# Optimization experiments

Hardware: AMD Instinct MI355X
Metric: run time of the kernel (lower is better)

Reference implementation:

```python
import jax, jax.numpy as jnp
import numpy as np

NB = 8  # num_blocks

def setup_inputs() -> dict:
    key = jax.random.key(0)
    ks = jax.random.split(key, 8)
    C = 128
    C8 = C // 8
    s = 0.05
    x = jax.random.normal(ks[0], (1, C, 64, 64, 64), dtype=jnp.float32)
    Wq = jax.random.normal(ks[1], (C8, C), dtype=jnp.float32) * s
    bq = jax.random.normal(ks[2], (C8,), dtype=jnp.float32) * s
    Wk = jax.random.normal(ks[3], (C8, C), dtype=jnp.float32) * s
    bk = jax.random.normal(ks[4], (C8,), dtype=jnp.float32) * s
    Wv = jax.random.normal(ks[5], (C, C), dtype=jnp.float32) * s
    bv = jax.random.normal(ks[6], (C,), dtype=jnp.float32) * s
    # torch inits gamma=0 (output == x, zero grads through attention);
    # use 0.5 so the attention path is actually exercised.
    gamma = jnp.full((1,), 0.5, dtype=jnp.float32)
    return dict(x=x, Wq=Wq, bq=bq, Wk=Wk, bk=bk, Wv=Wv, bv=bv, gamma=gamma)

def reference(x, Wq, bq, Wk, bk, Wv, bv, gamma):
    B, C, D, H, W = x.shape
    db, hb, wb = D // NB, H // NB, W // NB
    n = db * hb * wb
    # (i, j, k, B, C, db, hb, wb) block layout
    xr = x.reshape(B, C, NB, db, NB, hb, NB, wb).transpose(2, 4, 6, 0, 1, 3, 5, 7)
    ar = jnp.arange(NB)
    # NOTE: original code computes k = i % num_blocks, i.e. k == i always.
    # Only the (i, j, i) diagonal blocks are attended; the rest stay zero in `out`.
    blk = xr[ar, :, ar].reshape(NB * NB * B, C, n)  # (P, C, n), P = NB*NB*B
    # 1x1x1 convs == per-voxel linear layers over channels
    q = jnp.einsum('pcn,dc->pdn', blk, Wq) + bq[None, :, None]  # (P, C/8, n)
    k = jnp.einsum('pcn,dc->pdn', blk, Wk) + bk[None, :, None]  # (P, C/8, n)
    v = jnp.einsum('pcn,dc->pdn', blk, Wv) + bv[None, :, None]  # (P, C,   n)
    attn = jax.nn.softmax(jnp.einsum('pdn,pdm->pnm', q, k), axis=-1)  # (P, n_q, n_k)
    ob = jnp.einsum('pdm,pnm->pdn', v, attn)  # value @ attn^T, (P, C, n)
    ob = ob.reshape(NB, NB, B, C, db, hb, wb)
    out = jnp.zeros_like(xr).at[ar, :, ar].set(ob)  # only k==i diagonal filled
    out = out.transpose(3, 4, 0, 5, 1, 6, 2, 7).reshape(B, C, D, H, W)
    return gamma * out + x
```

## Files before the change

### kernel.cpp

```cpp
#include <hip/hip_runtime.h>

typedef __attribute__((ext_vector_type(8))) short bf16x8;
typedef __attribute__((ext_vector_type(4))) float f32x4;
typedef __attribute__((ext_vector_type(4))) int i32x4;
typedef __attribute__((ext_vector_type(4))) float float4v;

#define MFMA16(a, b, c) __builtin_amdgcn_mfma_f32_16x16x32_bf16((a), (b), (c), 0, 0, 0)

__device__ __forceinline__ unsigned short f2bf(float f) {
    unsigned u = __builtin_bit_cast(unsigned, f);
    u += 0x7fffu + ((u >> 16) & 1u);
    return (unsigned short)(u >> 16);
}
__device__ __forceinline__ float bf2f(unsigned short s) {
    unsigned u = ((unsigned)s) << 16;
    return __builtin_bit_cast(float, u);
}
__device__ __forceinline__ int pkbf(float a, float b) {
    return (int)f2bf(a) | ((int)f2bf(b) << 16);
}


__global__ __launch_bounds__(512, 2) void battn_kernel(
    const float* __restrict__ x,
    const float* __restrict__ Wq, const float* __restrict__ bq,
    const float* __restrict__ Wk, const float* __restrict__ bk,
    const float* __restrict__ Wv, const float* __restrict__ bv,
    const float* __restrict__ gamma, float* __restrict__ out)
{
    __shared__ __attribute__((aligned(128))) char smem[159744];
    const int bid = blockIdx.x;
    const int tid = threadIdx.x;

    if (bid >= 64) {
        const float4v* __restrict__ xin = (const float4v*)x;
        float4v* __restrict__ o4 = (float4v*)out;
        const int total = 1 << 23;
        for (int u = (bid - 64) * 512 + tid; u < total; u += 384 * 512) {
            if ((((u >> 1) ^ (u >> 13)) & 7) != 0) {
                o4[u] = xin[u];
            }
        }
        return;
    }

    const int p = bid;
    const int ib = p >> 3, jb = p & 7;
    const int vbase = ib * 8 * 4096 + jb * 8 * 64 + ib * 8;
    const int lane = tid & 63, wv = tid >> 6;
    const int g = lane >> 4, c15 = lane & 15;

    for (int it = 0; it < 32; ++it) {
        int ch = it * 512 + tid;
        int c = ch >> 7;
        int m = (ch & 127) * 4;
        int vox = ((m >> 6) << 12) + (((m >> 3) & 7) << 6) + (m & 7);
        float4v v = *(const float4v*)(x + c * 262144 + vbase + vox);
        char* bp = smem + ((m * 256 + 2 * c) ^ (((m >> 2) & 7) << 4));
        *(unsigned short*)(bp)       = f2bf(v[0]);
        *(unsigned short*)(bp + 256) = f2bf(v[1]);
        *(unsigned short*)(bp + 512) = f2bf(v[2]);
        *(unsigned short*)(bp + 768) = f2bf(v[3]);
    }

    bf16x8 wqf[4], wkf[4], wvf[4];
    #pragma unroll
    for (int ks = 0; ks < 4; ++ks) {
        const float* sq = Wq + c15 * 128 + ks * 32 + g * 8;
        const float* sk = Wk + c15 * 128 + ks * 32 + g * 8;
        const float* sv = Wv + (wv * 16 + c15) * 128 + ks * 32 + g * 8;
        #pragma unroll
        for (int e = 0; e < 8; ++e) {
            wqf[ks][e] = (short)f2bf(sq[e]);
            wkf[ks][e] = (short)f2bf(sk[e]);
            wvf[ks][e] = (short)f2bf(sv[e]);
        }
    }
    const float bqv = bq[c15], bkv = bk[c15];
    const f32x4 zacc = {0.f, 0.f, 0.f, 0.f};
    const bf16x8 zfrag = (bf16x8)(short)0;

    __syncthreads();

    #pragma unroll
    for (int qi = 0; qi < 4; ++qi) {
        f32x4 acc = zacc;
        int mrow = wv * 64 + qi * 16 + c15;
        int sw = ((mrow >> 2) & 7) << 4;
        #pragma unroll
        for (int ks = 0; ks < 4; ++ks) {
            bf16x8 af = *(const bf16x8*)(smem + ((mrow * 256 + ks * 64 + g * 16) ^ sw));
            acc = MFMA16(af, wqf[ks], acc);
        }
        #pragma unroll
        for (int r = 0; r < 4; ++r) {
            int nql = qi * 16 + g * 4 + r;
            *(unsigned short*)(smem + 131072 + wv * 2048 + nql * 32 + 2 * c15) = f2bf(acc[r] + bqv);
        }
    }
    __syncthreads();
    bf16x8 qf[4];
    #pragma unroll
    for (int t = 0; t < 4; ++t) {
        bf16x8 v = zfrag;
        if (g < 2) v = *(const bf16x8*)(smem + 131072 + wv * 2048 + (t * 16 + c15) * 32 + g * 16);
        qf[t] = v;
    }
    __syncthreads();

    #pragma unroll
    for (int qi = 0; qi < 4; ++qi) {
        f32x4 acc = zacc;
        int mrow = wv * 64 + qi * 16 + c15;
        int sw = ((mrow >> 2) & 7) << 4;
        #pragma unroll
        for (int ks = 0; ks < 4; ++ks) {
            bf16x8 af = *(const bf16x8*)(smem + ((mrow * 256 + ks * 64 + g * 16) ^ sw));
            acc = MFMA16(af, wkf[ks], acc);
        }
        #pragma unroll
        for (int r = 0; r < 4; ++r) {
            int mk = wv * 64 + qi * 16 + g * 4 + r;
            *(unsigned short*)(smem + 131072 + mk * 32 + 2 * c15) = f2bf(acc[r] + bkv);
        }
    }
    __syncthreads();

    f32x4 o[4][8];
    #pragma unroll
    for (int t = 0; t < 4; ++t)
        #pragma unroll
        for (int ci = 0; ci < 8; ++ci)
            o[t][ci] = zacc;
    float lsum[4] = {0.f, 0.f, 0.f, 0.f};

    for (int kt = 0; kt < 16; ++kt) {
        int mk0 = kt * 32;
        #pragma unroll
        for (int mi = 0; mi < 2; ++mi) {
            f32x4 acc = zacc;
            int mrow = mk0 + mi * 16 + c15;
            int sw = ((mrow >> 2) & 7) << 4;
            #pragma unroll
            for (int ks = 0; ks < 4; ++ks) {
                bf16x8 bf = *(const bf16x8*)(smem + ((mrow * 256 + ks * 64 + g * 16) ^ sw));
                acc = MFMA16(wvf[ks], bf, acc);
            }
            #pragma unroll
            for (int r = 0; r < 4; ++r) {
                int c_out = wv * 16 + g * 4 + r;
                *(unsigned short*)(smem + 147456 + c_out * 80 + 2 * (mi * 16 + c15)) = f2bf(acc[r]);
            }
        }
        __syncthreads();

        bf16x8 ka[2];
        #pragma unroll
        for (int ki = 0; ki < 2; ++ki) {
            bf16x8 v = zfrag;
            if (g < 2) v = *(const bf16x8*)(smem + 131072 + (mk0 + ki * 16 + c15) * 32 + g * 16);
            ka[ki] = v;
        }

        bf16x8 pa[4];
        #pragma unroll
        for (int t = 0; t < 4; ++t) {
            f32x4 s0 = MFMA16(ka[0], qf[t], zacc);
            f32x4 s1 = MFMA16(ka[1], qf[t], zacc);
            float e00 = __expf(s0[0]), e01 = __expf(s0[1]), e02 = __expf(s0[2]), e03 = __expf(s0[3]);
            float e10 = __expf(s1[0]), e11 = __expf(s1[1]), e12 = __expf(s1[2]), e13 = __expf(s1[3]);
            lsum[t] += (e00 + e01) + (e02 + e03) + ((e10 + e11) + (e12 + e13));
            int wA0 = pkbf(e00, e01), wB0 = pkbf(e02, e03);
            int wA1 = pkbf(e10, e11), wB1 = pkbf(e12, e13);
            int src1 = ((2 * g) & 3) * 16 + c15;
            int src2 = ((2 * g + 1) & 3) * 16 + c15;
            int sA0a = __shfl(wA0, src1, 64), sA1a = __shfl(wA1, src1, 64);
            int sB0a = __shfl(wB0, src1, 64), sB1a = __shfl(wB1, src1, 64);
            int sA0b = __shfl(wA0, src2, 64), sA1b = __shfl(wA1, src2, 64);
            int sB0b = __shfl(wB0, src2, 64), sB1b = __shfl(wB1, src2, 64);
            bool k1 = (g >= 2);
            i32x4 uu = { k1 ? sA1a : sA0a, k1 ? sB1a : sB0a,
                         k1 ? sA1b : sA0b, k1 ? sB1b : sB0b };
            pa[t] = __builtin_bit_cast(bf16x8, uu);
        }

        #pragma unroll
        for (int ci = 0; ci < 8; ++ci) {
            bf16x8 vb = *(const bf16x8*)(smem + 147456 + (ci * 16 + c15) * 80 + 16 * g);
            #pragma unroll
            for (int t = 0; t < 4; ++t)
                o[t][ci] = MFMA16(pa[t], vb, o[t][ci]);
        }
        __syncthreads();
    }

    #pragma unroll
    for (int t = 0; t < 4; ++t) {
        float l = lsum[t];
        l += __shfl_xor(l, 16, 64);
        l += __shfl_xor(l, 32, 64);
        if (g == 0)
            *(float*)(smem + 157696 + (wv * 64 + t * 16 + c15) * 4) = l;
    }

    #pragma unroll
    for (int t = 0; t < 4; ++t)
        #pragma unroll
        for (int ci = 0; ci < 8; ++ci)
            #pragma unroll
            for (int r = 0; r < 4; ++r) {
                int nq = wv * 64 + t * 16 + g * 4 + r;
                int c = ci * 16 + c15;
                *(unsigned short*)(smem + c * 1024 + 2 * (nq ^ ((c & 7) << 3))) = f2bf(o[t][ci][r]);
            }
    __syncthreads();

    float gma = gamma[0];
    float invl = 1.0f / *(const float*)(smem + 157696 + tid * 4);
    int vox = ((tid >> 6) << 12) + (((tid >> 3) & 7) << 6) + (tid & 7);
    int go = vbase + vox;
    for (int c = 0; c < 128; ++c) {
        float ov = bf2f(*(const unsigned short*)(smem + c * 1024 + 2 * (tid ^ ((c & 7) << 3))));
        int gidx = c * 262144 + go;
        out[gidx] = gma * (ov * invl + bv[c]) + x[gidx];
    }
}

extern "C" void kernel_launch(void* const* d_in, const int* in_sizes, int n_in,
                              void* d_out, int out_size, void* d_ws, size_t ws_size,
                              hipStream_t stream) {
    const float* x     = (const float*)d_in[0];
    const float* Wq    = (const float*)d_in[1];
    const float* bq    = (const float*)d_in[2];
    const float* Wk    = (const float*)d_in[3];
    const float* bk    = (const float*)d_in[4];
    const float* Wv    = (const float*)d_in[5];
    const float* bv    = (const float*)d_in[6];
    const float* gamma = (const float*)d_in[7];
    float* out = (float*)d_out;
    (void)in_sizes; (void)n_in; (void)out_size; (void)d_ws; (void)ws_size;
    battn_kernel<<<dim3(448), dim3(512), 0, stream>>>(x, Wq, bq, Wk, bk, Wv, bv, gamma, out);
}
```

Measured before the change: 105.8 us.

## Precompute V for whole block before attention loop and drop per-tile barriers

The V projection for all 512 keys is now computed up front into registers and written once to a swizzled shared-memory buffer that reuses the x region. This removes the per-tile V computation and its two barriers inside the 16-iteration attention loop, plus two barriers around the Q staging. The copy blocks now unroll four independent loads before the stores, and the grid grows from 448 to 512 blocks. In exchange, 32 f32x4 accumulators raise register pressure, which risks spilling at the 512-thread, 2-blocks-per-CU launch bounds.

```diff
diff --git a/kernel.cpp b/kernel.cpp
--- a/kernel.cpp
+++ b/kernel.cpp
@@ -20,6 +20,8 @@
     return (int)f2bf(a) | ((int)f2bf(b) << 16);
 }
 
+#define KOFF 131072
+#define LOFF 147456
 
 __global__ __launch_bounds__(512, 2) void battn_kernel(
     const float* __restrict__ x,
@@ -28,7 +30,7 @@
     const float* __restrict__ Wv, const float* __restrict__ bv,
     const float* __restrict__ gamma, float* __restrict__ out)
 {
-    __shared__ __attribute__((aligned(128))) char smem[159744];
+    __shared__ __attribute__((aligned(128))) char smem[149504];
     const int bid = blockIdx.x;
     const int tid = threadIdx.x;
 
@@ -36,11 +38,22 @@
         const float4v* __restrict__ xin = (const float4v*)x;
         float4v* __restrict__ o4 = (float4v*)out;
         const int total = 1 << 23;
-        for (int u = (bid - 64) * 512 + tid; u < total; u += 384 * 512) {
-            if ((((u >> 1) ^ (u >> 13)) & 7) != 0) {
-                o4[u] = xin[u];
-            }
-        }
+        const int T = (int)((gridDim.x - 64) << 9);
+        int u = ((bid - 64) << 9) + tid;
+#define PRED(v) (((((v) >> 1) ^ ((v) >> 13)) & 7) != 0)
+        for (; u + 3 * T < total; u += 4 * T) {
+            float4v a0 = xin[u];
+            float4v a1 = xin[u + T];
+            float4v a2 = xin[u + 2 * T];
+            float4v a3 = xin[u + 3 * T];
+            if (PRED(u)) o4[u] = a0;
+            if (PRED(u + T)) o4[u + T] = a1;
+            if (PRED(u + 2 * T)) o4[u + 2 * T] = a2;
+            if (PRED(u + 3 * T)) o4[u + 3 * T] = a3;
+        }
+        for (; u < total; u += T)
+            if (PRED(u)) o4[u] = xin[u];
+#undef PRED
         return;
     }
 
@@ -95,18 +108,16 @@
         #pragma unroll
         for (int r = 0; r < 4; ++r) {
             int nql = qi * 16 + g * 4 + r;
-            *(unsigned short*)(smem + 131072 + wv * 2048 + nql * 32 + 2 * c15) = f2bf(acc[r] + bqv);
-        }
-    }
-    __syncthreads();
+            *(unsigned short*)(smem + KOFF + wv * 2048 + nql * 32 + 2 * c15) = f2bf(acc[r] + bqv);
+        }
+    }
     bf16x8 qf[4];
     #pragma unroll
     for (int t = 0; t < 4; ++t) {
         bf16x8 v = zfrag;
-        if (g < 2) v = *(const bf16x8*)(smem + 131072 + wv * 2048 + (t * 16 + c15) * 32 + g * 16);
+        if (g < 2) v = *(const bf16x8*)(smem + KOFF + wv * 2048 + (t * 16 + c15) * 32 + g * 16);
         qf[t] = v;
     }
-    __syncthreads();
 
     #pragma unroll
     for (int qi = 0; qi < 4; ++qi) {
@@ -121,7 +132,32 @@
         #pragma unroll
         for (int r = 0; r < 4; ++r) {
             int mk = wv * 64 + qi * 16 + g * 4 + r;
-            *(unsigned short*)(smem + 131072 + mk * 32 + 2 * c15) = f2bf(acc[r] + bkv);
+            *(unsigned short*)(smem + KOFF + mk * 32 + 2 * c15) = f2bf(acc[r] + bkv);
+        }
+    }
+
+    f32x4 vacc[32];
+    #pragma unroll
+    for (int mt = 0; mt < 32; ++mt) vacc[mt] = zacc;
+    #pragma unroll
+    for (int mt = 0; mt < 32; ++mt) {
+        int mrow = mt * 16 + c15;
+        int sw = ((mrow >> 2) & 7) << 4;
+        #pragma unroll
+        for (int ks = 0; ks < 4; ++ks) {
+            bf16x8 bf = *(const bf16x8*)(smem + ((mrow * 256 + ks * 64 + g * 16) ^ sw));
+            vacc[mt] = MFMA16(wvf[ks], bf, vacc[mt]);
+        }
+    }
+    __syncthreads();
+
+    #pragma unroll
+    for (int mt = 0; mt < 32; ++mt) {
+        #pragma unroll
+        for (int r = 0; r < 4; ++r) {
+            int c_out = wv * 16 + g * 4 + r;
+            int mk = mt * 16 + c15;
+            *(unsigned short*)(smem + c_out * 1024 + ((2 * mk) ^ ((c_out & 7) << 4))) = f2bf(vacc[mt][r]);
         }
     }
     __syncthreads();
@@ -136,29 +172,11 @@
 
     for (int kt = 0; kt < 16; ++kt) {
         int mk0 = kt * 32;
-        #pragma unroll
-        for (int mi = 0; mi < 2; ++mi) {
-            f32x4 acc = zacc;
-            int mrow = mk0 + mi * 16 + c15;
-            int sw = ((mrow >> 2) & 7) << 4;
-            #pragma unroll
-            for (int ks = 0; ks < 4; ++ks) {
-                bf16x8 bf = *(const bf16x8*)(smem + ((mrow * 256 + ks * 64 + g * 16) ^ sw));
-                acc = MFMA16(wvf[ks], bf, acc);
-            }
-            #pragma unroll
-            for (int r = 0; r < 4; ++r) {
-                int c_out = wv * 16 + g * 4 + r;
-                *(unsigned short*)(smem + 147456 + c_out * 80 + 2 * (mi * 16 + c15)) = f2bf(acc[r]);
-            }
-        }
-        __syncthreads();
-
         bf16x8 ka[2];
         #pragma unroll
         for (int ki = 0; ki < 2; ++ki) {
             bf16x8 v = zfrag;
-            if (g < 2) v = *(const bf16x8*)(smem + 131072 + (mk0 + ki * 16 + c15) * 32 + g * 16);
+            if (g < 2) v = *(const bf16x8*)(smem + KOFF + (mk0 + ki * 16 + c15) * 32 + g * 16);
             ka[ki] = v;
         }
 
@@ -186,12 +204,12 @@
 
         #pragma unroll
         for (int ci = 0; ci < 8; ++ci) {
-            bf16x8 vb = *(const bf16x8*)(smem + 147456 + (ci * 16 + c15) * 80 + 16 * g);
+            int c = ci * 16 + c15;
+            bf16x8 vb = *(const bf16x8*)(smem + c * 1024 + ((mk0 * 2 + 16 * g) ^ ((c & 7) << 4)));
             #pragma unroll
             for (int t = 0; t < 4; ++t)
                 o[t][ci] = MFMA16(pa[t], vb, o[t][ci]);
         }
-        __syncthreads();
     }
 
     #pragma unroll
@@ -200,8 +218,10 @@
         l += __shfl_xor(l, 16, 64);
         l += __shfl_xor(l, 32, 64);
         if (g == 0)
-            *(float*)(smem + 157696 + (wv * 64 + t * 16 + c15) * 4) = l;
-    }
+            *(float*)(smem + LOFF + (wv * 64 + t * 16 + c15) * 4) = l;
+    }
+
+    __syncthreads();
 
     #pragma unroll
     for (int t = 0; t < 4; ++t)
@@ -211,16 +231,16 @@
             for (int r = 0; r < 4; ++r) {
                 int nq = wv * 64 + t * 16 + g * 4 + r;
                 int c = ci * 16 + c15;
-                *(unsigned short*)(smem + c * 1024 + 2 * (nq ^ ((c & 7) << 3))) = f2bf(o[t][ci][r]);
+                *(unsigned short*)(smem + c * 1024 + ((2 * nq) ^ ((c & 7) << 4))) = f2bf(o[t][ci][r]);
             }
     __syncthreads();
 
     float gma = gamma[0];
-    float invl = 1.0f / *(const float*)(smem + 157696 + tid * 4);
+    float invl = 1.0f / *(const float*)(smem + LOFF + tid * 4);
     int vox = ((tid >> 6) << 12) + (((tid >> 3) & 7) << 6) + (tid & 7);
     int go = vbase + vox;
     for (int c = 0; c < 128; ++c) {
-        float ov = bf2f(*(const unsigned short*)(smem + c * 1024 + 2 * (tid ^ ((c & 7) << 3))));
+        float ov = bf2f(*(const unsigned short*)(smem + c * 1024 + ((2 * tid) ^ ((c & 7) << 4))));
         int gidx = c * 262144 + go;
         out[gidx] = gma * (ov * invl + bv[c]) + x[gidx];
     }
@@ -239,5 +259,5 @@
     const float* gamma = (const float*)d_in[7];
     float* out = (float*)d_out;
     (void)in_sizes; (void)n_in; (void)out_size; (void)d_ws; (void)ws_size;
-    battn_kernel<<<dim3(448), dim3(512), 0, stream>>>(x, Wq, bq, Wk, bk, Wv, bv, gamma, out);
-}
+    battn_kernel<<<dim3(512), dim3(512), 0, stream>>>(x, Wq, bq, Wk, bk, Wv, bv, gamma, out);
+}
```

Result: slower. 110.8 us (+4.7%).
